# Optimization experiments

Measured on AMD Instinct MI355X. Metric: run time of the kernel, lower is better.

Reference implementation:

```python
import math
import jax, jax.numpy as jnp
import numpy as np

D_MODEL = 1024
NUM_HEADS = 16
HEAD_DIM = D_MODEL // NUM_HEADS
CAUSAL = True


def setup_inputs() -> dict:
    key = jax.random.key(0)
    ks = jax.random.split(key, 9)
    B, S = 2, 2048
    s = 1.0 / math.sqrt(D_MODEL)
    x = jax.random.normal(ks[0], (B, S, D_MODEL), dtype=jnp.float32)
    Wq = jax.random.normal(ks[1], (D_MODEL, D_MODEL), dtype=jnp.float32) * s
    bq = jax.random.normal(ks[2], (D_MODEL,), dtype=jnp.float32) * 0.01
    Wk = jax.random.normal(ks[3], (D_MODEL, D_MODEL), dtype=jnp.float32) * s
    bk = jax.random.normal(ks[4], (D_MODEL,), dtype=jnp.float32) * 0.01
    Wv = jax.random.normal(ks[5], (D_MODEL, D_MODEL), dtype=jnp.float32) * s
    bv = jax.random.normal(ks[6], (D_MODEL,), dtype=jnp.float32) * 0.01
    Wo = jax.random.normal(ks[7], (D_MODEL, D_MODEL), dtype=jnp.float32) * s
    bo = jax.random.normal(ks[8], (D_MODEL,), dtype=jnp.float32) * 0.01
    return {"x": x, "Wq": Wq, "bq": bq, "Wk": Wk, "bk": bk,
            "Wv": Wv, "bv": bv, "Wo": Wo, "bo": bo}


def reference(x, Wq, bq, Wk, bk, Wv, bv, Wo, bo):
    B, S, _ = x.shape
    # projections (torch Linear: x @ W.T + b; here W already stored as [in,out])
    q = x @ Wq + bq
    k = x @ Wk + bk
    v = x @ Wv + bv
    # split heads -> [B, H, S, hd]
    def split(t):
        return t.reshape(B, S, NUM_HEADS, HEAD_DIM).transpose(0, 2, 1, 3)
    q, k, v = split(q), split(k), split(v)
    scores = jnp.einsum('bhqd,bhkd->bhqk', q, k) / math.sqrt(HEAD_DIM)
    if CAUSAL:
        causal = jnp.tril(jnp.ones((S, S), dtype=bool))  # True = keep
        scores = jnp.where(causal, scores, -jnp.inf)
    attn = jax.nn.softmax(scores, axis=-1)
    out = jnp.einsum('bhqk,bhkd->bhqd', attn, v)
    out = out.transpose(0, 2, 1, 3).reshape(B, S, D_MODEL)
    return out @ Wo + bo
```

## Files before the change

### kernel.cpp

```cpp
#include <hip/hip_runtime.h>
#include <hip/hip_bf16.h>

typedef __bf16 bf16_t;
typedef __bf16 v8bf __attribute__((ext_vector_type(8)));
typedef float  v4f  __attribute__((ext_vector_type(4)));

#define MFMA16(a, b, c) __builtin_amdgcn_mfma_f32_16x16x32_bf16((a), (b), (c), 0, 0, 0)

#define GLDS16(g, l) __builtin_amdgcn_global_load_lds(                         \
    (const __attribute__((address_space(1))) void*)(g),                        \
    (__attribute__((address_space(3))) void*)(l), 16, 0, 0)

#define B_SZ   2
#define SEQ    2048
#define DM     1024
#define NH     16
#define HD     64
#define M_TOT  4096

#define QSCALE 0.18033688011112043f

__global__ __launch_bounds__(256)
void conv_x_kernel(const float* __restrict__ src, bf16_t* __restrict__ dst)
{
    int i = (blockIdx.x * 256 + threadIdx.x) * 8;
    float4 a = *reinterpret_cast<const float4*>(src + i);
    float4 b = *reinterpret_cast<const float4*>(src + i + 4);
    union { bf16_t h[8]; int4 v; } u;
    u.h[0] = (bf16_t)a.x; u.h[1] = (bf16_t)a.y; u.h[2] = (bf16_t)a.z; u.h[3] = (bf16_t)a.w;
    u.h[4] = (bf16_t)b.x; u.h[5] = (bf16_t)b.y; u.h[6] = (bf16_t)b.z; u.h[7] = (bf16_t)b.w;
    *reinterpret_cast<int4*>(dst + i) = u.v;
}

__global__ __launch_bounds__(256)
void conv_wt_kernel(const float* __restrict__ Wq, const float* __restrict__ Wk,
                    const float* __restrict__ Wv, const float* __restrict__ Wo,
                    bf16_t* __restrict__ WqkvT, bf16_t* __restrict__ WoT)
{
    __shared__ float t[32][33];
    const int z = blockIdx.z;
    const float* src = (z == 0) ? Wq : (z == 1) ? Wk : (z == 2) ? Wv : Wo;
    bf16_t* dst = (z < 3) ? (WqkvT + (size_t)z * 1048576) : WoT;
    const int tx = threadIdx.x & 31, ty = threadIdx.x >> 5;
    const int c0 = blockIdx.x * 32, r0 = blockIdx.y * 32;
#pragma unroll
    for (int i = 0; i < 4; ++i)
        t[ty + i * 8][tx] = src[(size_t)(r0 + ty + i * 8) * DM + c0 + tx];
    __syncthreads();
#pragma unroll
    for (int i = 0; i < 4; ++i)
        dst[(size_t)(c0 + ty + i * 8) * DM + r0 + tx] = (bf16_t)t[tx][ty + i * 8];
}

__global__ __launch_bounds__(256)
void gemm_qkv_kernel(const bf16_t* __restrict__ A, const bf16_t* __restrict__ BT,
                     const float* __restrict__ b0, const float* __restrict__ b1,
                     const float* __restrict__ b2,
                     bf16_t* __restrict__ oQ, bf16_t* __restrict__ oK,
                     bf16_t* __restrict__ oV)
{
    __shared__ __align__(16) bf16_t As[2 * 128 * 64];
    __shared__ __align__(16) bf16_t Bs[2 * 128 * 64];

    const int tid  = threadIdx.x;
    const int lane = tid & 63;
    const int wave = tid >> 6;
    const int wm   = (wave >> 1) * 64;
    const int wn   = (wave & 1) * 64;
    const int quad = lane >> 4;
    const int l15  = lane & 15;
    const int l7   = l15 & 7;

    const int mat = blockIdx.x >> 3;
    const int n0  = (blockIdx.x & 7) * 128;
    const int m0  = blockIdx.y * 128;
    const bf16_t* Bmat = BT + (size_t)mat * 1048576;

    const bf16_t *ap[4], *bp[4];
#pragma unroll
    for (int i = 0; i < 4; ++i) {
        int cidx = (wave * 4 + i) * 64 + lane;
        int r = cidx >> 3;
        int c = (cidx & 7) ^ (r & 7);
        ap[i] = A    + (size_t)(m0 + r) * DM + c * 8;
        bp[i] = Bmat + (size_t)(n0 + r) * DM + c * 8;
    }

    const v4f vzero = {0.f, 0.f, 0.f, 0.f};
    v4f acc[4][4];
#pragma unroll
    for (int mt = 0; mt < 4; ++mt)
#pragma unroll
        for (int nt = 0; nt < 4; ++nt) acc[mt][nt] = vzero;

#pragma unroll
    for (int i = 0; i < 4; ++i) {
        GLDS16(ap[i], As + (wave * 4 + i) * 512);
        GLDS16(bp[i], Bs + (wave * 4 + i) * 512);
        ap[i] += 64; bp[i] += 64;
    }

    for (int it = 0; it < 16; ++it) {
        const int cur = it & 1, nxt = cur ^ 1;
        __syncthreads();
        if (it < 15) {
#pragma unroll
            for (int i = 0; i < 4; ++i) {
                GLDS16(ap[i], As + nxt * 8192 + (wave * 4 + i) * 512);
                GLDS16(bp[i], Bs + nxt * 8192 + (wave * 4 + i) * 512);
                ap[i] += 64; bp[i] += 64;
            }
        }
#pragma unroll
        for (int ks = 0; ks < 2; ++ks) {
            v8bf af[4], bfq[4];
#pragma unroll
            for (int mt = 0; mt < 4; ++mt)
                af[mt] = *reinterpret_cast<const v8bf*>(
                    &As[cur * 8192 + (wm + mt * 16 + l15) * 64 + ((ks * 4 + quad) ^ l7) * 8]);
#pragma unroll
            for (int nt = 0; nt < 4; ++nt)
                bfq[nt] = *reinterpret_cast<const v8bf*>(
                    &Bs[cur * 8192 + (wn + nt * 16 + l15) * 64 + ((ks * 4 + quad) ^ l7) * 8]);
#pragma unroll
            for (int mt = 0; mt < 4; ++mt)
#pragma unroll
                for (int nt = 0; nt < 4; ++nt)
                    acc[mt][nt] = MFMA16(bfq[nt], af[mt], acc[mt][nt]);
        }
    }

    const float* bias = (mat == 0) ? b0 : (mat == 1) ? b1 : b2;
    if (mat != 2) {
        bf16_t* dst = (mat == 0) ? oQ : oK;
        const float scale = (mat == 0) ? QSCALE : 1.0f;
        const int h = (n0 + wn) >> 6;
#pragma unroll
        for (int nt = 0; nt < 4; ++nt) {
            const int dbase = nt * 16 + quad * 4;
            float4 bv = *reinterpret_cast<const float4*>(bias + n0 + wn + dbase);
#pragma unroll
            for (int mt = 0; mt < 4; ++mt) {
                int srow = m0 + wm + mt * 16 + l15;
                int b = srow >> 11, s = srow & 2047;
                union { bf16_t hh[4]; int2 v; } u;
                u.hh[0] = (bf16_t)((acc[mt][nt][0] + bv.x) * scale);
                u.hh[1] = (bf16_t)((acc[mt][nt][1] + bv.y) * scale);
                u.hh[2] = (bf16_t)((acc[mt][nt][2] + bv.z) * scale);
                u.hh[3] = (bf16_t)((acc[mt][nt][3] + bv.w) * scale);
                *reinterpret_cast<int2*>(
                    dst + ((size_t)(b * NH + h) * SEQ + s) * HD + dbase) = u.v;
            }
        }
    } else {
#pragma unroll
        for (int nt = 0; nt < 4; ++nt) {
#pragma unroll
            for (int r = 0; r < 4; ++r) {
                int coln = n0 + wn + nt * 16 + quad * 4 + r;
                float bv = bias[coln];
                int h = coln >> 6, d = coln & 63;
#pragma unroll
                for (int mt = 0; mt < 4; ++mt) {
                    int srow = m0 + wm + mt * 16 + l15;
                    int b = srow >> 11, s = srow & 2047;
                    oV[((size_t)(b * NH + h) * HD + d) * SEQ + s] =
                        (bf16_t)(acc[mt][nt][r] + bv);
                }
            }
        }
    }
}

__global__ __launch_bounds__(256)
void gemm_o_kernel(const bf16_t* __restrict__ A, const bf16_t* __restrict__ BT,
                   const float* __restrict__ bias, float* __restrict__ out)
{
    __shared__ __align__(16) bf16_t As[2 * 128 * 64];
    __shared__ __align__(16) bf16_t Bs[2 * 64 * 64];

    const int tid  = threadIdx.x;
    const int lane = tid & 63;
    const int wave = tid >> 6;
    const int wm   = (wave >> 1) * 64;
    const int wn   = (wave & 1) * 32;
    const int quad = lane >> 4;
    const int l15  = lane & 15;
    const int l7   = l15 & 7;

    const int n0 = blockIdx.x * 64;
    const int m0 = blockIdx.y * 128;

    const bf16_t *ap[4], *bp[2];
#pragma unroll
    for (int i = 0; i < 4; ++i) {
        int cidx = (wave * 4 + i) * 64 + lane;
        int r = cidx >> 3;
        int c = (cidx & 7) ^ (r & 7);
        ap[i] = A + (size_t)(m0 + r) * DM + c * 8;
    }
#pragma unroll
    for (int i = 0; i < 2; ++i) {
        int cidx = (wave * 2 + i) * 64 + lane;
        int r = cidx >> 3;
        int c = (cidx & 7) ^ (r & 7);
        bp[i] = BT + (size_t)(n0 + r) * DM + c * 8;
    }

    const v4f vzero = {0.f, 0.f, 0.f, 0.f};
    v4f acc[4][2];
#pragma unroll
    for (int mt = 0; mt < 4; ++mt)
#pragma unroll
        for (int nt = 0; nt < 2; ++nt) acc[mt][nt] = vzero;

#pragma unroll
    for (int i = 0; i < 4; ++i) { GLDS16(ap[i], As + (wave * 4 + i) * 512); ap[i] += 64; }
#pragma unroll
    for (int i = 0; i < 2; ++i) { GLDS16(bp[i], Bs + (wave * 2 + i) * 512); bp[i] += 64; }

    for (int it = 0; it < 16; ++it) {
        const int cur = it & 1, nxt = cur ^ 1;
        __syncthreads();
        if (it < 15) {
#pragma unroll
            for (int i = 0; i < 4; ++i) {
                GLDS16(ap[i], As + nxt * 8192 + (wave * 4 + i) * 512);
                ap[i] += 64;
            }
#pragma unroll
            for (int i = 0; i < 2; ++i) {
                GLDS16(bp[i], Bs + nxt * 4096 + (wave * 2 + i) * 512);
                bp[i] += 64;
            }
        }
#pragma unroll
        for (int ks = 0; ks < 2; ++ks) {
            v8bf af[4], bfq[2];
#pragma unroll
            for (int mt = 0; mt < 4; ++mt)
                af[mt] = *reinterpret_cast<const v8bf*>(
                    &As[cur * 8192 + (wm + mt * 16 + l15) * 64 + ((ks * 4 + quad) ^ l7) * 8]);
#pragma unroll
            for (int nt = 0; nt < 2; ++nt)
                bfq[nt] = *reinterpret_cast<const v8bf*>(
                    &Bs[cur * 4096 + (wn + nt * 16 + l15) * 64 + ((ks * 4 + quad) ^ l7) * 8]);
#pragma unroll
            for (int mt = 0; mt < 4; ++mt)
#pragma unroll
                for (int nt = 0; nt < 2; ++nt)
                    acc[mt][nt] = MFMA16(af[mt], bfq[nt], acc[mt][nt]);
        }
    }

#pragma unroll
    for (int mt = 0; mt < 4; ++mt) {
#pragma unroll
        for (int nt = 0; nt < 2; ++nt) {
            int col = n0 + wn + nt * 16 + l15;
            float bv = bias[col];
#pragma unroll
            for (int r = 0; r < 4; ++r) {
                int row = m0 + wm + mt * 16 + quad * 4 + r;
                out[(size_t)row * DM + col] = acc[mt][nt][r] + bv;
            }
        }
    }
}

__global__ __launch_bounds__(256)
void attn_kernel(const bf16_t* __restrict__ Q, const bf16_t* __restrict__ K,
                 const bf16_t* __restrict__ Vt, bf16_t* __restrict__ O)
{
    __shared__ __align__(16) bf16_t Ks[64 * 64];
    __shared__ __align__(16) bf16_t Vs[64 * 64];
    __shared__ __align__(16) bf16_t Ps[64 * 72];

    const int tid  = threadIdx.x;
    const int lane = tid & 63;
    const int w    = tid >> 6;
    const int quad = lane >> 4;
    const int l15  = lane & 15;
    const int l7   = lane & 7;

    const int x = blockIdx.x, y = blockIdx.y;
    const int u_ = (x + (y & 24)) & 31;
    const int r_ = u_ >> 3, s_ = u_ & 7;
    const int t  = (r_ == 0) ? s_ : (r_ == 1) ? 31 - s_ : (r_ == 2) ? 8 + s_ : 23 - s_;
    const int bh = y;
    const int q0 = t * 64;
    const size_t base = (size_t)bh * SEQ * HD;

    const bf16_t* Qg = Q  + base;
    const bf16_t* Kg = K  + base;
    const bf16_t* Vg = Vt + base;

    v8bf qf[2];
    {
        const bf16_t* qrow = Qg + (size_t)(q0 + w * 16 + l15) * HD;
        qf[0] = *reinterpret_cast<const v8bf*>(qrow + quad * 8);
        qf[1] = *reinterpret_cast<const v8bf*>(qrow + 32 + quad * 8);
    }

    const int rr0 = tid >> 3;
    const int cc0 = (tid & 7) ^ (rr0 & 7);
    const bf16_t* kp0 = Kg + (size_t)rr0 * HD + cc0 * 8;
    const bf16_t* kp1 = kp0 + 32 * HD;
    const bf16_t* vp0 = Vg + (size_t)rr0 * SEQ + cc0 * 8;
    const bf16_t* vp1 = vp0 + (size_t)32 * SEQ;
    bf16_t* dK0 = Ks + w * 512;          bf16_t* dK1 = Ks + 2048 + w * 512;
    bf16_t* dV0 = Vs + w * 512;          bf16_t* dV1 = Vs + 2048 + w * 512;

    const v4f vzero = {0.f, 0.f, 0.f, 0.f};
    v4f acc_o[4];
#pragma unroll
    for (int dt = 0; dt < 4; ++dt) acc_o[dt] = vzero;
    float lrow = 0.f;
    const int qg = q0 + w * 16 + l15;

    for (int kt = 0; kt <= t; ++kt) {
        GLDS16(kp0, dK0);  GLDS16(kp1, dK1);
        GLDS16(vp0, dV0);  GLDS16(vp1, dV1);
        kp0 += 64 * HD;  kp1 += 64 * HD;  vp0 += 64;  vp1 += 64;
        __syncthreads();

        v4f st[4];
#pragma unroll
        for (int ktile = 0; ktile < 4; ++ktile) st[ktile] = vzero;
#pragma unroll
        for (int ks = 0; ks < 2; ++ks) {
            v8bf kb[4];
#pragma unroll
            for (int ktile = 0; ktile < 4; ++ktile)
                kb[ktile] = *reinterpret_cast<const v8bf*>(
                    &Ks[(ktile * 16 + l15) * 64 + ((ks * 4 + quad) ^ l7) * 8]);
#pragma unroll
            for (int ktile = 0; ktile < 4; ++ktile)
                st[ktile] = MFMA16(kb[ktile], qf[ks], st[ktile]);
        }

        const bool diagI = (kt == t);
        float rs = 0.f;
        const int prow = (w * 16 + l15) * 72;
#pragma unroll
        for (int ktile = 0; ktile < 4; ++ktile) {
            union { bf16_t h[4]; int2 v; } u;
            if (diagI && ktile > w) {
                u.v.x = 0; u.v.y = 0;
            } else if (diagI && ktile == w) {
#pragma unroll
                for (int r = 0; r < 4; ++r) {
                    int kg = kt * 64 + ktile * 16 + quad * 4 + r;
                    float p = (kg > qg) ? 0.f : exp2f(st[ktile][r]);
                    rs += p;
                    u.h[r] = (bf16_t)p;
                }
            } else {
#pragma unroll
                for (int r = 0; r < 4; ++r) {
                    float p = exp2f(st[ktile][r]);
                    rs += p;
                    u.h[r] = (bf16_t)p;
                }
            }
            *reinterpret_cast<int2*>(&Ps[prow + ktile * 16 + quad * 4]) = u.v;
        }
        rs += __shfl_xor(rs, 16);
        rs += __shfl_xor(rs, 32);
        lrow += rs;

#pragma unroll
        for (int ks = 0; ks < 2; ++ks) {
            v8bf vb[4];
#pragma unroll
            for (int dt = 0; dt < 4; ++dt)
                vb[dt] = *reinterpret_cast<const v8bf*>(
                    &Vs[(dt * 16 + l15) * 64 + ((ks * 4 + quad) ^ l7) * 8]);
            v8bf pf = *reinterpret_cast<const v8bf*>(
                &Ps[(w * 16 + l15) * 72 + ks * 32 + quad * 8]);
#pragma unroll
            for (int dt = 0; dt < 4; ++dt)
                acc_o[dt] = MFMA16(vb[dt], pf, acc_o[dt]);
        }
        __syncthreads();
    }

    const int bO = bh >> 4, hO = bh & 15;
    float rinv = 1.f / lrow;
    int s = q0 + w * 16 + l15;
#pragma unroll
    for (int dt = 0; dt < 4; ++dt) {
        union { bf16_t h[4]; int2 v; } u;
#pragma unroll
        for (int r = 0; r < 4; ++r)
            u.h[r] = (bf16_t)(acc_o[dt][r] * rinv);
        *reinterpret_cast<int2*>(
            &O[((size_t)bO * SEQ + s) * DM + hO * 64 + dt * 16 + quad * 4]) = u.v;
    }
}

extern "C" void kernel_launch(void* const* d_in, const int* in_sizes, int n_in,
                              void* d_out, int out_size, void* d_ws, size_t ws_size,
                              hipStream_t stream) {
    const float* x  = (const float*)d_in[0];
    const float* Wq = (const float*)d_in[1];
    const float* bq = (const float*)d_in[2];
    const float* Wk = (const float*)d_in[3];
    const float* bk = (const float*)d_in[4];
    const float* Wv = (const float*)d_in[5];
    const float* bv = (const float*)d_in[6];
    const float* Wo = (const float*)d_in[7];
    const float* bo = (const float*)d_in[8];

    bf16_t* ws = (bf16_t*)d_ws;
    bf16_t* xb     = ws;
    bf16_t* WqkvT  = ws + 4194304;
    bf16_t* WoT    = ws + 7340032;
    bf16_t* Qb     = ws + 8388608;
    bf16_t* Kb     = ws + 12582912;
    bf16_t* Vb     = ws + 16777216;
    bf16_t* Ob     = ws;

    conv_x_kernel<<<2048, 256, 0, stream>>>(x, xb);
    conv_wt_kernel<<<dim3(32, 32, 4), 256, 0, stream>>>(Wq, Wk, Wv, Wo, WqkvT, WoT);
    gemm_qkv_kernel<<<dim3(24, 32), 256, 0, stream>>>(xb, WqkvT, bq, bk, bv, Qb, Kb, Vb);
    attn_kernel<<<dim3(32, 32), 256, 0, stream>>>(Qb, Kb, Vb, Ob);
    gemm_o_kernel<<<dim3(16, 32), 256, 0, stream>>>(Ob, WoT, bo, (float*)d_out);
}
```

Before: 199.4 us.

## Double-buffer K/V tiles and pair causal query tiles per attention block

The attention kernel now double-buffers the K and V shared-memory tiles, so the next tile's global-to-LDS load is issued while the current tile is being computed. It also drops one barrier per iteration. Each block now processes two query tiles, p and 31-p, one after the other, which evens out causal work per block and halves the grid. exp2f is replaced with the hardware exp2 builtin. The cost is double the K/V LDS footprint, which may lower occupancy, and half as many blocks to spread across CUs.

```diff
diff --git a/kernel.cpp b/kernel.cpp
--- a/kernel.cpp
+++ b/kernel.cpp
@@ -272,8 +272,8 @@
 void attn_kernel(const bf16_t* __restrict__ Q, const bf16_t* __restrict__ K,
                  const bf16_t* __restrict__ Vt, bf16_t* __restrict__ O)
 {
-    __shared__ __align__(16) bf16_t Ks[64 * 64];
-    __shared__ __align__(16) bf16_t Vs[64 * 64];
+    __shared__ __align__(16) bf16_t Ks[2][64 * 64];
+    __shared__ __align__(16) bf16_t Vs[2][64 * 64];
     __shared__ __align__(16) bf16_t Ps[64 * 72];
 
     const int tid  = threadIdx.x;
@@ -283,119 +283,129 @@
     const int l15  = lane & 15;
     const int l7   = lane & 7;
 
-    const int x = blockIdx.x, y = blockIdx.y;
-    const int u_ = (x + (y & 24)) & 31;
-    const int r_ = u_ >> 3, s_ = u_ & 7;
-    const int t  = (r_ == 0) ? s_ : (r_ == 1) ? 31 - s_ : (r_ == 2) ? 8 + s_ : 23 - s_;
-    const int bh = y;
-    const int q0 = t * 64;
+    const int p  = blockIdx.x;
+    const int bh = blockIdx.y;
     const size_t base = (size_t)bh * SEQ * HD;
-
     const bf16_t* Qg = Q  + base;
     const bf16_t* Kg = K  + base;
     const bf16_t* Vg = Vt + base;
 
-    v8bf qf[2];
-    {
-        const bf16_t* qrow = Qg + (size_t)(q0 + w * 16 + l15) * HD;
-        qf[0] = *reinterpret_cast<const v8bf*>(qrow + quad * 8);
-        qf[1] = *reinterpret_cast<const v8bf*>(qrow + 32 + quad * 8);
-    }
-
     const int rr0 = tid >> 3;
     const int cc0 = (tid & 7) ^ (rr0 & 7);
-    const bf16_t* kp0 = Kg + (size_t)rr0 * HD + cc0 * 8;
-    const bf16_t* kp1 = kp0 + 32 * HD;
-    const bf16_t* vp0 = Vg + (size_t)rr0 * SEQ + cc0 * 8;
-    const bf16_t* vp1 = vp0 + (size_t)32 * SEQ;
-    bf16_t* dK0 = Ks + w * 512;          bf16_t* dK1 = Ks + 2048 + w * 512;
-    bf16_t* dV0 = Vs + w * 512;          bf16_t* dV1 = Vs + 2048 + w * 512;
-
+    const int bO = bh >> 4, hO = bh & 15;
     const v4f vzero = {0.f, 0.f, 0.f, 0.f};
-    v4f acc_o[4];
-#pragma unroll
-    for (int dt = 0; dt < 4; ++dt) acc_o[dt] = vzero;
-    float lrow = 0.f;
-    const int qg = q0 + w * 16 + l15;
-
-    for (int kt = 0; kt <= t; ++kt) {
-        GLDS16(kp0, dK0);  GLDS16(kp1, dK1);
-        GLDS16(vp0, dV0);  GLDS16(vp1, dV1);
+
+    for (int phase = 0; phase < 2; ++phase) {
+        const int t  = phase ? (31 - p) : p;
+        const int q0 = t * 64;
+        const int qg = q0 + w * 16 + l15;
+
+        v8bf qf[2];
+        {
+            const bf16_t* qrow = Qg + (size_t)qg * HD;
+            qf[0] = *reinterpret_cast<const v8bf*>(qrow + quad * 8);
+            qf[1] = *reinterpret_cast<const v8bf*>(qrow + 32 + quad * 8);
+        }
+
+        const bf16_t* kp0 = Kg + (size_t)rr0 * HD + cc0 * 8;
+        const bf16_t* kp1 = kp0 + 32 * HD;
+        const bf16_t* vp0 = Vg + (size_t)rr0 * SEQ + cc0 * 8;
+        const bf16_t* vp1 = vp0 + (size_t)32 * SEQ;
+
+        v4f acc_o[4];
+#pragma unroll
+        for (int dt = 0; dt < 4; ++dt) acc_o[dt] = vzero;
+        float lrow = 0.f;
+
+        __syncthreads();
+        GLDS16(kp0, &Ks[0][w * 512]);
+        GLDS16(kp1, &Ks[0][2048 + w * 512]);
+        GLDS16(vp0, &Vs[0][w * 512]);
+        GLDS16(vp1, &Vs[0][2048 + w * 512]);
         kp0 += 64 * HD;  kp1 += 64 * HD;  vp0 += 64;  vp1 += 64;
-        __syncthreads();
-
-        v4f st[4];
-#pragma unroll
-        for (int ktile = 0; ktile < 4; ++ktile) st[ktile] = vzero;
-#pragma unroll
-        for (int ks = 0; ks < 2; ++ks) {
-            v8bf kb[4];
-#pragma unroll
-            for (int ktile = 0; ktile < 4; ++ktile)
-                kb[ktile] = *reinterpret_cast<const v8bf*>(
-                    &Ks[(ktile * 16 + l15) * 64 + ((ks * 4 + quad) ^ l7) * 8]);
-#pragma unroll
-            for (int ktile = 0; ktile < 4; ++ktile)
-                st[ktile] = MFMA16(kb[ktile], qf[ks], st[ktile]);
-        }
-
-        const bool diagI = (kt == t);
-        float rs = 0.f;
-        const int prow = (w * 16 + l15) * 72;
-#pragma unroll
-        for (int ktile = 0; ktile < 4; ++ktile) {
+
+        for (int kt = 0; kt <= t; ++kt) {
+            const int cur = kt & 1, nxt = cur ^ 1;
+            __syncthreads();
+            if (kt < t) {
+                GLDS16(kp0, &Ks[nxt][w * 512]);
+                GLDS16(kp1, &Ks[nxt][2048 + w * 512]);
+                GLDS16(vp0, &Vs[nxt][w * 512]);
+                GLDS16(vp1, &Vs[nxt][2048 + w * 512]);
+                kp0 += 64 * HD;  kp1 += 64 * HD;  vp0 += 64;  vp1 += 64;
+            }
+
+            v4f st[4];
+#pragma unroll
+            for (int ktile = 0; ktile < 4; ++ktile) st[ktile] = vzero;
+#pragma unroll
+            for (int ks = 0; ks < 2; ++ks) {
+                v8bf kb[4];
+#pragma unroll
+                for (int ktile = 0; ktile < 4; ++ktile)
+                    kb[ktile] = *reinterpret_cast<const v8bf*>(
+                        &Ks[cur][(ktile * 16 + l15) * 64 + ((ks * 4 + quad) ^ l7) * 8]);
+#pragma unroll
+                for (int ktile = 0; ktile < 4; ++ktile)
+                    st[ktile] = MFMA16(kb[ktile], qf[ks], st[ktile]);
+            }
+
+            const bool diagI = (kt == t);
+            float rs = 0.f;
+            const int prow = (w * 16 + l15) * 72;
+#pragma unroll
+            for (int ktile = 0; ktile < 4; ++ktile) {
+                union { bf16_t h[4]; int2 v; } u;
+                if (diagI && ktile > w) {
+                    u.v.x = 0; u.v.y = 0;
+                } else if (diagI && ktile == w) {
+#pragma unroll
+                    for (int r = 0; r < 4; ++r) {
+                        int kg = kt * 64 + ktile * 16 + quad * 4 + r;
+                        float pv = (kg > qg) ? 0.f : __builtin_amdgcn_exp2f(st[ktile][r]);
+                        rs += pv;
+                        u.h[r] = (bf16_t)pv;
+                    }
+                } else {
+#pragma unroll
+                    for (int r = 0; r < 4; ++r) {
+                        float pv = __builtin_amdgcn_exp2f(st[ktile][r]);
+                        rs += pv;
+                        u.h[r] = (bf16_t)pv;
+                    }
+                }
+                *reinterpret_cast<int2*>(&Ps[prow + ktile * 16 + quad * 4]) = u.v;
+            }
+            rs += __shfl_xor(rs, 16);
+            rs += __shfl_xor(rs, 32);
+            lrow += rs;
+
+#pragma unroll
+            for (int ks = 0; ks < 2; ++ks) {
+                v8bf vb[4];
+#pragma unroll
+                for (int dt = 0; dt < 4; ++dt)
+                    vb[dt] = *reinterpret_cast<const v8bf*>(
+                        &Vs[cur][(dt * 16 + l15) * 64 + ((ks * 4 + quad) ^ l7) * 8]);
+                v8bf pf = *reinterpret_cast<const v8bf*>(
+                    &Ps[(w * 16 + l15) * 72 + ks * 32 + quad * 8]);
+#pragma unroll
+                for (int dt = 0; dt < 4; ++dt)
+                    acc_o[dt] = MFMA16(vb[dt], pf, acc_o[dt]);
+            }
+        }
+
+        float rinv = 1.f / lrow;
+        int s = q0 + w * 16 + l15;
+#pragma unroll
+        for (int dt = 0; dt < 4; ++dt) {
             union { bf16_t h[4]; int2 v; } u;
-            if (diagI && ktile > w) {
-                u.v.x = 0; u.v.y = 0;
-            } else if (diagI && ktile == w) {
-#pragma unroll
-                for (int r = 0; r < 4; ++r) {
-                    int kg = kt * 64 + ktile * 16 + quad * 4 + r;
-                    float p = (kg > qg) ? 0.f : exp2f(st[ktile][r]);
-                    rs += p;
-                    u.h[r] = (bf16_t)p;
-                }
-            } else {
-#pragma unroll
-                for (int r = 0; r < 4; ++r) {
-                    float p = exp2f(st[ktile][r]);
-                    rs += p;
-                    u.h[r] = (bf16_t)p;
-                }
-            }
-            *reinterpret_cast<int2*>(&Ps[prow + ktile * 16 + quad * 4]) = u.v;
-        }
-        rs += __shfl_xor(rs, 16);
-        rs += __shfl_xor(rs, 32);
-        lrow += rs;
-
-#pragma unroll
-        for (int ks = 0; ks < 2; ++ks) {
-            v8bf vb[4];
-#pragma unroll
-            for (int dt = 0; dt < 4; ++dt)
-                vb[dt] = *reinterpret_cast<const v8bf*>(
-                    &Vs[(dt * 16 + l15) * 64 + ((ks * 4 + quad) ^ l7) * 8]);
-            v8bf pf = *reinterpret_cast<const v8bf*>(
-                &Ps[(w * 16 + l15) * 72 + ks * 32 + quad * 8]);
-#pragma unroll
-            for (int dt = 0; dt < 4; ++dt)
-                acc_o[dt] = MFMA16(vb[dt], pf, acc_o[dt]);
-        }
-        __syncthreads();
-    }
-
-    const int bO = bh >> 4, hO = bh & 15;
-    float rinv = 1.f / lrow;
-    int s = q0 + w * 16 + l15;
-#pragma unroll
-    for (int dt = 0; dt < 4; ++dt) {
-        union { bf16_t h[4]; int2 v; } u;
-#pragma unroll
-        for (int r = 0; r < 4; ++r)
-            u.h[r] = (bf16_t)(acc_o[dt][r] * rinv);
-        *reinterpret_cast<int2*>(
-            &O[((size_t)bO * SEQ + s) * DM + hO * 64 + dt * 16 + quad * 4]) = u.v;
+#pragma unroll
+            for (int r = 0; r < 4; ++r)
+                u.h[r] = (bf16_t)(acc_o[dt][r] * rinv);
+            *reinterpret_cast<int2*>(
+                &O[((size_t)bO * SEQ + s) * DM + hO * 64 + dt * 16 + quad * 4]) = u.v;
+        }
     }
 }
 
@@ -424,6 +434,6 @@
     conv_x_kernel<<<2048, 256, 0, stream>>>(x, xb);
     conv_wt_kernel<<<dim3(32, 32, 4), 256, 0, stream>>>(Wq, Wk, Wv, Wo, WqkvT, WoT);
     gemm_qkv_kernel<<<dim3(24, 32), 256, 0, stream>>>(xb, WqkvT, bq, bk, bv, Qb, Kb, Vb);
-    attn_kernel<<<dim3(32, 32), 256, 0, stream>>>(Qb, Kb, Vb, Ob);
+    attn_kernel<<<dim3(16, 32), 256, 0, stream>>>(Qb, Kb, Vb, Ob);
     gemm_o_kernel<<<dim3(16, 32), 256, 0, stream>>>(Ob, WoT, bo, (float*)d_out);
 }
```

New measurement: 195.0 us. 2.2% less time.
